# Kernel optimization log

Hardware: AMD Instinct MI355X
Metric: run time of the kernel (lower is better)

Reference implementation:

```python
import jax, jax.numpy as jnp
import numpy as np

B, S, E, H, LD, P, NC = 4, 256, 256, 8, 128, 256, 2
N = S * P  # total points (static)
EPS = 1e-5


def setup_inputs() -> dict:
    key = jax.random.key(0)
    ks = jax.random.split(key, 12)
    r = lambda i, shape, s: jax.random.normal(ks[i], shape, jnp.float32) * s
    return dict(
        gl_feats=jax.random.normal(ks[0], (S, B, E), jnp.float32),
        lo_feats=jax.random.normal(ks[1], (B, N, LD), jnp.float32),
        centroids=jax.random.normal(ks[2], (B, S, 2), jnp.float32),
        np_cluster=jnp.full((S,), P, jnp.int32),
        fc1_w=r(3, (16, 2), 0.5), fc1_b=jnp.zeros(16, jnp.float32),
        fc2_w=r(4, (E, 16), 0.1), fc2_b=jnp.zeros(E, jnp.float32),
        in_proj_w=r(5, (3 * E, E), 0.05), in_proj_b=jnp.zeros(3 * E, jnp.float32),
        out_proj_w=r(6, (E, E), 0.05), out_proj_b=jnp.zeros(E, jnp.float32),
        conv2_w=r(7, (E // 2, LD + E), 0.05), conv2_b=jnp.zeros(E // 2, jnp.float32),
        bn2_gamma=jnp.ones(E // 2, jnp.float32), bn2_beta=jnp.zeros(E // 2, jnp.float32),
        bn2_mean=jnp.zeros(E // 2, jnp.float32), bn2_var=jnp.ones(E // 2, jnp.float32),
        conv3_w=r(8, (64, E // 2), 0.05), conv3_b=jnp.zeros(64, jnp.float32),
        bn3_gamma=jnp.ones(64, jnp.float32), bn3_beta=jnp.zeros(64, jnp.float32),
        bn3_mean=jnp.zeros(64, jnp.float32), bn3_var=jnp.ones(64, jnp.float32),
        conv4_w=r(9, (NC, 64), 0.05), conv4_b=jnp.zeros(NC, jnp.float32),
    )


def _bn(z, g, b, m, v):
    # inference-mode BatchNorm1d over the channel (last) axis
    return (z - m) * jax.lax.rsqrt(v + EPS) * g + b


def reference(gl_feats, lo_feats, centroids, np_cluster,
              fc1_w, fc1_b, fc2_w, fc2_b,
              in_proj_w, in_proj_b, out_proj_w, out_proj_b,
              conv2_w, conv2_b, bn2_gamma, bn2_beta, bn2_mean, bn2_var,
              conv3_w, conv3_b, bn3_gamma, bn3_beta, bn3_mean, bn3_var,
              conv4_w, conv4_b):
    # positional encoding of centroids: Linear(2,16) -> leaky_relu -> Linear(16,E)
    h = centroids @ fc1_w.T + fc1_b                      # [B,S,16]
    h = jnp.where(h >= 0, h, 0.01 * h)                   # leaky_relu_, slope 0.01
    pos = h @ fc2_w.T + fc2_b                            # [B,S,E]
    x = gl_feats.transpose(1, 0, 2) + pos                # [B,S,E] (torch MHA is seq-first)

    # MultiheadAttention (self-attn, eval-mode dropout=identity)
    qkv = x @ in_proj_w.T + in_proj_b                    # [B,S,3E]
    q, k, v = jnp.split(qkv, 3, axis=-1)
    dh = E // H
    qh = q.reshape(B, S, H, dh)
    kh = k.reshape(B, S, H, dh)
    vh = v.reshape(B, S, H, dh)
    scores = jnp.einsum('bqhd,bkhd->bhqk', qh, kh) * (1.0 / np.sqrt(dh))
    attn = jax.nn.softmax(scores, axis=-1)               # [B,H,S,S]
    ctx = jnp.einsum('bhqk,bkhd->bqhd', attn, vh).reshape(B, S, E)
    attn_out = ctx @ out_proj_w.T + out_proj_b           # [B,S,E]

    # segment-broadcast: replace the python repeat/cat loop with a gather
    cluster_ids = jnp.repeat(jnp.arange(S), np_cluster, total_repeat_length=N)  # [N]
    global_feat = attn_out[:, cluster_ids, :]            # [B,N,E]

    pc = jnp.concatenate([lo_feats, global_feat], axis=2)  # [B,N,LD+E]
    # 1x1 Conv1d == pointwise Linear over channels
    h2 = jax.nn.relu(_bn(pc @ conv2_w.T + conv2_b, bn2_gamma, bn2_beta, bn2_mean, bn2_var))
    h3 = jax.nn.relu(_bn(h2 @ conv3_w.T + conv3_b, bn3_gamma, bn3_beta, bn3_mean, bn3_var))
    out = h3 @ conv4_w.T + conv4_b                       # [B,N,NC]
    return out.transpose(0, 2, 1)                        # [B,NC,N] to match torch layout
```

## Files before the change

### kernel.cpp

```cpp
#include <hip/hip_runtime.h>

#define B_   4
#define S_   256
#define E_   256
#define H_   8
#define LD_  128
#define N_   65536
#define NC_  2

typedef __attribute__((ext_vector_type(8))) short s8v;
typedef __attribute__((ext_vector_type(4))) float f32x4;

__device__ __forceinline__ short f2bf(float f) {
  unsigned u;
  asm("v_cvt_pk_bf16_f32 %0, %1, %2" : "=v"(u) : "v"(f), "v"(f));
  return (short)u;
}
__device__ __forceinline__ float bf2f(short s) {
  union { float f; unsigned u; } v; v.u = ((unsigned)(unsigned short)s) << 16;
  return v.f;
}
__device__ __forceinline__ s8v pack8(float4 a, float4 b) {
  union { s8v s; unsigned u[4]; } r;
  asm("v_cvt_pk_bf16_f32 %0, %1, %2" : "=v"(r.u[0]) : "v"(a.x), "v"(a.y));
  asm("v_cvt_pk_bf16_f32 %0, %1, %2" : "=v"(r.u[1]) : "v"(a.z), "v"(a.w));
  asm("v_cvt_pk_bf16_f32 %0, %1, %2" : "=v"(r.u[2]) : "v"(b.x), "v"(b.y));
  asm("v_cvt_pk_bf16_f32 %0, %1, %2" : "=v"(r.u[3]) : "v"(b.z), "v"(b.w));
  return r.s;
}

__global__ __launch_bounds__(256) void prep_k(
    const int* __restrict__ npc, int* __restrict__ ids,
    const float* __restrict__ ipw, const float* __restrict__ opw,
    const float* __restrict__ opb,
    const float* __restrict__ w2, const float* __restrict__ w3,
    const float* __restrict__ b2, const float* __restrict__ g2,
    const float* __restrict__ be2, const float* __restrict__ mu2,
    const float* __restrict__ va2,
    const float* __restrict__ b3, const float* __restrict__ g3,
    const float* __restrict__ be3, const float* __restrict__ mu3,
    const float* __restrict__ va3,
    short* __restrict__ iph, short* __restrict__ ipl,
    short* __restrict__ Mh, short* __restrict__ Ml,
    float* __restrict__ g0v,
    short* __restrict__ w2p, short* __restrict__ w3p,
    float* __restrict__ sc2, float* __restrict__ sh2,
    float* __restrict__ sc3, float* __restrict__ sh3,
    const float* __restrict__ gl, const float* __restrict__ cen,
    const float* __restrict__ fc1w, const float* __restrict__ fc1b,
    const float* __restrict__ fc2w, const float* __restrict__ fc2b,
    short* __restrict__ Xhi, short* __restrict__ Xlo) {
  __shared__ int red[256];
  __shared__ float hsh[16];
  __shared__ float wrow[256];
  __shared__ float gred[256];
  int bid = blockIdx.x, t = threadIdx.x;
  if (bid < 768) {
    int i = bid * 256 + t;
    if (i < 196608) {
      float v = ipw[i]; short h = f2bf(v);
      iph[i] = h; ipl[i] = f2bf(v - bf2f(h));
    }
    if (i < 16384) {
      int g = i >> 9, l2 = (i >> 3) & 63, j = i & 7;
      int chh = g >> 4, ct = (g >> 2) & 3, ks = g & 3;
      int row = 64 * chh + 16 * ct + (l2 & 15);
      int col = ks * 32 + (l2 >> 4) * 8 + j;
      w2p[i] = f2bf(w2[row * 384 + col]);
    }
    if (i < 8192) {
      int g = i >> 9, l2 = (i >> 3) & 63, j = i & 7;
      int ct = g >> 2, ks = g & 3;
      int row = 16 * ct + (l2 & 15);
      int col = ks * 32 + (l2 >> 4) * 8 + j;
      w3p[i] = f2bf(w3[row * 128 + col]);
    }
    if (i < 128) {
      float sc = g2[i] * rsqrtf(va2[i] + 1e-5f);
      sc2[i] = sc; sh2[i] = (b2[i] - mu2[i]) * sc + be2[i];
    }
    if (i < 64) {
      float sc = g3[i] * rsqrtf(va3[i] + 1e-5f);
      sc3[i] = sc; sh3[i] = (b3[i] - mu3[i]) * sc + be3[i];
    }
  } else if (bid <= 1024) {
    int s = bid - 768;
    int val = (s == 256) ? npc[t] : ((t < s) ? npc[t] : 0);
    red[t] = val;
    __syncthreads();
    for (int off = 128; off > 0; off >>= 1) {
      if (t < off) red[t] += red[t + off];
      __syncthreads();
    }
    int st = red[0];
    if (s < 256) {
      int en = st + npc[s]; if (en > N_) en = N_;
      for (int n = st + t; n < en; n += 256) ids[n] = s;
    } else {
      for (int n = st + t; n < N_; n += 256) ids[n] = 255;
    }
  } else if (bid <= 2048) {
    int bs = bid - 1025;
    int b = bs >> 8, s = bs & 255;
    if (t < 16) {
      float c0 = cen[bs * 2 + 0], c1 = cen[bs * 2 + 1];
      float v = c0 * fc1w[2 * t] + c1 * fc1w[2 * t + 1] + fc1b[t];
      hsh[t] = (v >= 0.f) ? v : 0.01f * v;
    }
    __syncthreads();
    float p = fc2b[t];
#pragma unroll
    for (int j = 0; j < 16; j++) p += hsh[j] * fc2w[t * 16 + j];
    float v = gl[((size_t)s * B_ + b) * E_ + t] + p;
    short h = f2bf(v);
    Xhi[(size_t)bs * E_ + t] = h;
    Xlo[(size_t)bs * E_ + t] = f2bf(v - bf2f(h));
  } else {
    int c = bid - 2049;
    wrow[t] = w2[c * 384 + 128 + t];
    gred[t] = 0.f;
    __syncthreads();
    float acc = 0.f;
#pragma unroll 8
    for (int k = 0; k < 256; k++) acc += wrow[k] * opw[(size_t)k * 256 + t];
    short h = f2bf(acc);
    Mh[(size_t)c * 256 + t] = h;
    Ml[(size_t)c * 256 + t] = f2bf(acc - bf2f(h));
    gred[t] = wrow[t] * opb[t];
    __syncthreads();
    for (int off = 128; off > 0; off >>= 1) {
      if (t < off) gred[t] += gred[t + off];
      __syncthreads();
    }
    if (t == 0) g0v[c] = gred[0];
  }
}

__global__ __launch_bounds__(256) void gemm_x3_k(
    const short* __restrict__ Ah, const short* __restrict__ Al,
    const short* __restrict__ Wh, const short* __restrict__ Wl,
    const float* __restrict__ bias, float* __restrict__ Cf,
    int M, int N, int K) {
  __shared__ __align__(16) short gs[18432];
  const int AH = 0, AL = 4608, WH = 9216, WL = 13824;
  int t = threadIdx.x;
  int row0 = blockIdx.x * 64, col0 = blockIdx.y * 64;
  int w = t >> 6, l = t & 63, quad = l >> 4, lr = l & 15;
  int m0 = w * 16;
  int ar = t >> 2, aq = (t & 3) * 16;
  f32x4 acc[4];
#pragma unroll
  for (int i = 0; i < 4; i++) acc[i] = (f32x4)(0.f);

  for (int kc = 0; kc < K; kc += 64) {
    __syncthreads();
    {
      size_t ra = (size_t)(row0 + ar) * K + kc + aq;
      size_t rw = (size_t)(col0 + ar) * K + kc + aq;
      *(s8v*)&gs[AH + ar * 72 + aq]     = *(const s8v*)&Ah[ra];
      *(s8v*)&gs[AH + ar * 72 + aq + 8] = *(const s8v*)&Ah[ra + 8];
      *(s8v*)&gs[AL + ar * 72 + aq]     = *(const s8v*)&Al[ra];
      *(s8v*)&gs[AL + ar * 72 + aq + 8] = *(const s8v*)&Al[ra + 8];
      *(s8v*)&gs[WH + ar * 72 + aq]     = *(const s8v*)&Wh[rw];
      *(s8v*)&gs[WH + ar * 72 + aq + 8] = *(const s8v*)&Wh[rw + 8];
      *(s8v*)&gs[WL + ar * 72 + aq]     = *(const s8v*)&Wl[rw];
      *(s8v*)&gs[WL + ar * 72 + aq + 8] = *(const s8v*)&Wl[rw + 8];
    }
    __syncthreads();
#pragma unroll
    for (int ks = 0; ks < 2; ks++) {
      int ko = ks * 32 + quad * 8;
      s8v ah = *(const s8v*)&gs[AH + (m0 + lr) * 72 + ko];
      s8v al = *(const s8v*)&gs[AL + (m0 + lr) * 72 + ko];
#pragma unroll
      for (int ct = 0; ct < 4; ct++) {
        s8v bh = *(const s8v*)&gs[WH + (ct * 16 + lr) * 72 + ko];
        s8v bl = *(const s8v*)&gs[WL + (ct * 16 + lr) * 72 + ko];
        acc[ct] = __builtin_amdgcn_mfma_f32_16x16x32_bf16(ah, bh, acc[ct], 0, 0, 0);
        acc[ct] = __builtin_amdgcn_mfma_f32_16x16x32_bf16(al, bh, acc[ct], 0, 0, 0);
        acc[ct] = __builtin_amdgcn_mfma_f32_16x16x32_bf16(ah, bl, acc[ct], 0, 0, 0);
      }
    }
  }
#pragma unroll
  for (int ct = 0; ct < 4; ct++) {
    int c = col0 + ct * 16 + lr;
    float bb = bias[c];
#pragma unroll
    for (int rg = 0; rg < 4; rg++) {
      int r = row0 + m0 + quad * 4 + rg;
      Cf[(size_t)r * N + c] = acc[ct][rg] + bb;
    }
  }
}

__global__ __launch_bounds__(256) void gk_k(
    const short* __restrict__ Ah, const short* __restrict__ Al,
    const short* __restrict__ Wh, const short* __restrict__ Wl,
    const float* __restrict__ g0v, float* __restrict__ G) {
  __shared__ __align__(16) short gs[13824];
  const int AH = 0, AL = 4608, WH = 9216, WL = 11520;
  int t = threadIdx.x;
  int row0 = blockIdx.x * 64, col0 = blockIdx.y * 32;
  int w = t >> 6, l = t & 63, quad = l >> 4, lr = l & 15;
  int m0 = w * 16;
  int ar = t >> 2, aq = (t & 3) * 16;
  int wr = t >> 3, wq = (t & 7) * 8;
  f32x4 acc[2];
#pragma unroll
  for (int i = 0; i < 2; i++) acc[i] = (f32x4)(0.f);

  for (int kc = 0; kc < 256; kc += 64) {
    __syncthreads();
    {
      size_t ra = (size_t)(row0 + ar) * 256 + kc + aq;
      size_t rw = (size_t)(col0 + wr) * 256 + kc + wq;
      *(s8v*)&gs[AH + ar * 72 + aq]     = *(const s8v*)&Ah[ra];
      *(s8v*)&gs[AH + ar * 72 + aq + 8] = *(const s8v*)&Ah[ra + 8];
      *(s8v*)&gs[AL + ar * 72 + aq]     = *(const s8v*)&Al[ra];
      *(s8v*)&gs[AL + ar * 72 + aq + 8] = *(const s8v*)&Al[ra + 8];
      *(s8v*)&gs[WH + wr * 72 + wq]     = *(const s8v*)&Wh[rw];
      *(s8v*)&gs[WL + wr * 72 + wq]     = *(const s8v*)&Wl[rw];
    }
    __syncthreads();
#pragma unroll
    for (int ks = 0; ks < 2; ks++) {
      int ko = ks * 32 + quad * 8;
      s8v ah = *(const s8v*)&gs[AH + (m0 + lr) * 72 + ko];
      s8v al = *(const s8v*)&gs[AL + (m0 + lr) * 72 + ko];
#pragma unroll
      for (int ct = 0; ct < 2; ct++) {
        s8v bh = *(const s8v*)&gs[WH + (ct * 16 + lr) * 72 + ko];
        s8v bl = *(const s8v*)&gs[WL + (ct * 16 + lr) * 72 + ko];
        acc[ct] = __builtin_amdgcn_mfma_f32_16x16x32_bf16(ah, bh, acc[ct], 0, 0, 0);
        acc[ct] = __builtin_amdgcn_mfma_f32_16x16x32_bf16(al, bh, acc[ct], 0, 0, 0);
        acc[ct] = __builtin_amdgcn_mfma_f32_16x16x32_bf16(ah, bl, acc[ct], 0, 0, 0);
      }
    }
  }
#pragma unroll
  for (int ct = 0; ct < 2; ct++) {
    int c = col0 + ct * 16 + lr;
    float bb = g0v[c];
#pragma unroll
    for (int rg = 0; rg < 4; rg++) {
      int r = row0 + m0 + quad * 4 + rg;
      G[(size_t)r * 128 + c] = acc[ct][rg] + bb;
    }
  }
}

__global__ __launch_bounds__(256) void attn_k(const float* __restrict__ qkv,
                                              short* __restrict__ Chi,
                                              short* __restrict__ Clo) {
  int bid = blockIdx.x;
  int qt = bid & 7, h = (bid >> 3) & 7, b = bid >> 6;
  __shared__ __align__(16) float smem[16384];
  float* Kx = smem;
  float* Vx = smem + 8192;
  int t = threadIdx.x;
#pragma unroll
  for (int i = 0; i < 8; i++) {
    int row = i * 32 + (t >> 3);
    int d4 = (t & 7) * 4;
    const float* base = qkv + (size_t)(b * S_ + row) * 768 + h * 32 + d4;
    *(float4*)&Kx[row * 32 + d4] = *(const float4*)(base + 256);
    *(float4*)&Vx[row * 32 + d4] = *(const float4*)(base + 512);
  }
  int r = t & 31, g = t >> 5;
  float q[32];
  {
    const float* qb = qkv + (size_t)(b * S_ + qt * 32 + r) * 768 + h * 32;
#pragma unroll
    for (int d4 = 0; d4 < 32; d4 += 4) {
      float4 v = *(const float4*)(qb + d4);
      q[d4] = v.x; q[d4 + 1] = v.y; q[d4 + 2] = v.z; q[d4 + 3] = v.w;
    }
  }
  __syncthreads();
  const float scale = 0.17677669529663687f;
  int kk0 = g * 32;
  float sc[32];
  float m = -1e30f;
#pragma unroll
  for (int kk = 0; kk < 32; kk++) {
    const float* kr = &Kx[(kk0 + kk) * 32];
    float4 a = (float4){0.f, 0.f, 0.f, 0.f};
#pragma unroll
    for (int d4 = 0; d4 < 32; d4 += 4) {
      float4 kv = *(const float4*)(kr + d4);
      a.x += q[d4] * kv.x; a.y += q[d4 + 1] * kv.y;
      a.z += q[d4 + 2] * kv.z; a.w += q[d4 + 3] * kv.w;
    }
    float s = ((a.x + a.y) + (a.z + a.w)) * scale;
    sc[kk] = s;
    m = fmaxf(m, s);
  }
  float lsum = 0.f;
  float ctx[32];
#pragma unroll
  for (int d = 0; d < 32; d++) ctx[d] = 0.f;
#pragma unroll
  for (int kk = 0; kk < 32; kk++) {
    const float* vr = &Vx[(kk0 + kk) * 32];
    float p = __expf(sc[kk] - m);
    lsum += p;
#pragma unroll
    for (int d4 = 0; d4 < 32; d4 += 4) {
      float4 vv = *(const float4*)(vr + d4);
      ctx[d4] += p * vv.x; ctx[d4 + 1] += p * vv.y;
      ctx[d4 + 2] += p * vv.z; ctx[d4 + 3] += p * vv.w;
    }
  }
  __syncthreads();
  float* ctxbuf = smem;
  float* mbuf = smem + 8192;
  float* lbuf = smem + 8448;
  mbuf[g * 32 + r] = m;
  lbuf[g * 32 + r] = lsum;
#pragma unroll
  for (int d = 0; d < 32; d++)
    ctxbuf[(g * 32 + r) * 32 + ((d + r) & 31)] = ctx[d];
  __syncthreads();
  int r2 = t & 31, dq = t >> 5;
  float M = -1e30f;
#pragma unroll
  for (int gg = 0; gg < 8; gg++) M = fmaxf(M, mbuf[gg * 32 + r2]);
  float wg[8]; float L = 0.f;
#pragma unroll
  for (int gg = 0; gg < 8; gg++) {
    wg[gg] = __expf(mbuf[gg * 32 + r2] - M);
    L += lbuf[gg * 32 + r2] * wg[gg];
  }
  float invL = 1.f / L;
  size_t base = (size_t)(b * S_ + qt * 32 + r2) * E_ + h * 32;
#pragma unroll
  for (int dd = 0; dd < 4; dd++) {
    int d = dq * 4 + dd;
    float o = 0.f;
#pragma unroll
    for (int gg = 0; gg < 8; gg++)
      o += ctxbuf[(gg * 32 + r2) * 32 + ((d + r2) & 31)] * wg[gg];
    o *= invL;
    short hi = f2bf(o);
    Chi[base + d] = hi;
    Clo[base + d] = f2bf(o - bf2f(hi));
  }
}

__global__ __launch_bounds__(256, 4) void conv_fused_k(
    const float* __restrict__ lo, const float* __restrict__ G,
    const int* __restrict__ ids,
    const short* __restrict__ w2p, const short* __restrict__ w3p,
    const float* __restrict__ sc2, const float* __restrict__ sh2,
    const float* __restrict__ sc3, const float* __restrict__ sh3,
    const float* __restrict__ w4, const float* __restrict__ b4,
    float* __restrict__ out) {
  __shared__ __align__(16) short smem[17408];
  __shared__ int lds_ids[128];
  int t = threadIdx.x;
  int bid = blockIdx.x;
  int b = bid >> 9;
  int n0 = (bid & 511) << 7;
  int w = t >> 6, l = t & 63;
  int quad = l >> 4, lr = l & 15;
  int mh = w & 1, chh = w >> 1;
  int ar = t >> 1, akh = (t & 1) * 64;
  const float* lob = &lo[((size_t)b * N_ + n0 + ar) * LD_ + akh];

  int id0 = ids[n0], id127 = ids[n0 + 127];
  bool uni = (id0 == id127);
  float gseed[4];
  {
    const float* gr = &G[((size_t)b * 256 + id0) * 128 + 64 * chh + lr];
#pragma unroll
    for (int ct = 0; ct < 4; ct++) gseed[ct] = gr[16 * ct];
  }
  if (t < 128) lds_ids[t] = ids[n0 + t];

  {
    float4 pf[8];
#pragma unroll
    for (int j = 0; j < 8; j++) pf[j] = *(const float4*)(lob + j * 4);
#pragma unroll
    for (int j = 0; j < 4; j++)
      *(s8v*)&smem[ar * 136 + akh + j * 8] = pack8(pf[2 * j], pf[2 * j + 1]);
#pragma unroll
    for (int j = 0; j < 8; j++) pf[j] = *(const float4*)(lob + 32 + j * 4);
#pragma unroll
    for (int j = 0; j < 4; j++)
      *(s8v*)&smem[ar * 136 + akh + 32 + j * 8] = pack8(pf[2 * j], pf[2 * j + 1]);
  }
  __syncthreads();

  f32x4 acc2[4][4];
  if (uni) {
#pragma unroll
    for (int mt = 0; mt < 4; mt++)
#pragma unroll
      for (int ct = 0; ct < 4; ct++)
#pragma unroll
        for (int rg = 0; rg < 4; rg++)
          acc2[mt][ct][rg] = gseed[ct];
  } else {
#pragma unroll
    for (int mt = 0; mt < 4; mt++)
#pragma unroll
      for (int rg = 0; rg < 4; rg++) {
        int p = 64 * mh + 16 * mt + 4 * quad + rg;
        const float* gr = &G[((size_t)b * 256 + lds_ids[p]) * 128 + 64 * chh + lr];
#pragma unroll
        for (int ct = 0; ct < 4; ct++)
          acc2[mt][ct][rg] = gr[16 * ct];
      }
  }

#pragma unroll
  for (int ks = 0; ks < 4; ks++) {
    int ko = ks * 32 + quad * 8;
    s8v af[4], bfr[4];
#pragma unroll
    for (int mt = 0; mt < 4; mt++)
      af[mt] = *(const s8v*)&smem[(64 * mh + 16 * mt + lr) * 136 + ko];
#pragma unroll
    for (int ct = 0; ct < 4; ct++)
      bfr[ct] = *(const s8v*)&w2p[(((chh * 4 + ct) * 4 + ks) << 9) + l * 8];
#pragma unroll
    for (int mt = 0; mt < 4; mt++)
#pragma unroll
      for (int ct = 0; ct < 4; ct++)
        acc2[mt][ct] = __builtin_amdgcn_mfma_f32_16x16x32_bf16(af[mt], bfr[ct], acc2[mt][ct], 0, 0, 0);
  }
  __syncthreads();

#pragma unroll
  for (int ct = 0; ct < 4; ct++) {
    int c = 64 * chh + 16 * ct + lr;
    float sc = sc2[c], sh = sh2[c];
#pragma unroll
    for (int mt = 0; mt < 4; mt++)
#pragma unroll
      for (int rg = 0; rg < 4; rg++) {
        int p = 64 * mh + 16 * mt + 4 * quad + rg;
        float z = acc2[mt][ct][rg] * sc + sh;
        smem[p * 136 + c] = f2bf(fmaxf(z, 0.f));
      }
  }
  __syncthreads();

  f32x4 acc3[2][4];
#pragma unroll
  for (int i = 0; i < 2; i++)
#pragma unroll
    for (int j = 0; j < 4; j++) acc3[i][j] = (f32x4)(0.f);
#pragma unroll
  for (int ks = 0; ks < 4; ks++) {
    int ko = ks * 32 + quad * 8;
    s8v af2[2], bf3[4];
#pragma unroll
    for (int mt = 0; mt < 2; mt++)
      af2[mt] = *(const s8v*)&smem[(32 * w + 16 * mt + lr) * 136 + ko];
#pragma unroll
    for (int ct = 0; ct < 4; ct++)
      bf3[ct] = *(const s8v*)&w3p[(((ct * 4) + ks) << 9) + l * 8];
#pragma unroll
    for (int mt = 0; mt < 2; mt++)
#pragma unroll
      for (int ct = 0; ct < 4; ct++)
        acc3[mt][ct] = __builtin_amdgcn_mfma_f32_16x16x32_bf16(af2[mt], bf3[ct], acc3[mt][ct], 0, 0, 0);
  }

  float w4c0[4], w4c1[4], s3[4], b3sh[4];
#pragma unroll
  for (int ct = 0; ct < 4; ct++) {
    int c = 16 * ct + lr;
    s3[ct] = sc3[c]; b3sh[ct] = sh3[c];
    w4c0[ct] = w4[c];
    w4c1[ct] = w4[64 + c];
  }
  int c4s = lr & 1, rgs = (lr >> 1) & 3, mts = lr >> 3;
  float myout = 0.f;
#pragma unroll
  for (int mt = 0; mt < 2; mt++)
#pragma unroll
    for (int rg = 0; rg < 4; rg++) {
      float p0 = 0.f, p1 = 0.f;
#pragma unroll
      for (int ct = 0; ct < 4; ct++) {
        float z = fmaxf(fmaf(acc3[mt][ct][rg], s3[ct], b3sh[ct]), 0.f);
        p0 = fmaf(z, w4c0[ct], p0);
        p1 = fmaf(z, w4c1[ct], p1);
      }
#pragma unroll
      for (int m = 1; m < 16; m <<= 1) {
        p0 += __shfl_xor(p0, m, 64);
        p1 += __shfl_xor(p1, m, 64);
      }
      bool mine = (mt == mts) && (rg == rgs);
      float pv = c4s ? p1 : p0;
      myout = mine ? pv : myout;
    }
  {
    int p = 32 * w + 16 * mts + 4 * quad + rgs;
    out[((size_t)b * NC_ + c4s) * N_ + n0 + p] = myout + b4[c4s];
  }
}

extern "C" void kernel_launch(void* const* d_in, const int* in_sizes, int n_in,
                              void* d_out, int out_size, void* d_ws, size_t ws_size,
                              hipStream_t stream) {
  const float* gl   = (const float*)d_in[0];
  const float* lo   = (const float*)d_in[1];
  const float* cen  = (const float*)d_in[2];
  const int*   npc  = (const int*)d_in[3];
  const float* fc1w = (const float*)d_in[4];
  const float* fc1b = (const float*)d_in[5];
  const float* fc2w = (const float*)d_in[6];
  const float* fc2b = (const float*)d_in[7];
  const float* ipw  = (const float*)d_in[8];
  const float* ipb  = (const float*)d_in[9];
  const float* opw  = (const float*)d_in[10];
  const float* opb  = (const float*)d_in[11];
  const float* w2   = (const float*)d_in[12];
  const float* b2   = (const float*)d_in[13];
  const float* g2   = (const float*)d_in[14];
  const float* be2  = (const float*)d_in[15];
  const float* mu2  = (const float*)d_in[16];
  const float* va2  = (const float*)d_in[17];
  const float* w3   = (const float*)d_in[18];
  const float* b3   = (const float*)d_in[19];
  const float* g3   = (const float*)d_in[20];
  const float* be3  = (const float*)d_in[21];
  const float* mu3  = (const float*)d_in[22];
  const float* va3  = (const float*)d_in[23];
  const float* w4   = (const float*)d_in[24];
  const float* b4   = (const float*)d_in[25];

  char* ws = (char*)d_ws;
  float* qkv  = (float*)(ws);
  short* Xhi  = (short*)(ws + 3145728);
  short* Xlo  = (short*)(ws + 3670016);
  short* Chi  = (short*)(ws + 4194304);
  short* Clo  = (short*)(ws + 4718592);
  float* G    = (float*)(ws + 5242880);
  short* iph  = (short*)(ws + 5767168);
  short* ipl  = (short*)(ws + 6160384);
  short* Mh   = (short*)(ws + 6553600);
  short* Ml   = (short*)(ws + 6684672);
  short* w2p  = (short*)(ws + 6815744);
  short* w3p  = (short*)(ws + 6914048);
  int*   ids  = (int*)  (ws + 6930432);
  float* sc2  = (float*)(ws + 7192576);
  float* sh2  = (float*)(ws + 7193088);
  float* sc3  = (float*)(ws + 7193600);
  float* sh3  = (float*)(ws + 7193856);
  float* g0v  = (float*)(ws + 7194112);
  float* out  = (float*)d_out;

  prep_k<<<2177, 256, 0, stream>>>(npc, ids, ipw, opw, opb, w2, w3,
                                   b2, g2, be2, mu2, va2,
                                   b3, g3, be3, mu3, va3,
                                   iph, ipl, Mh, Ml, g0v, w2p, w3p,
                                   sc2, sh2, sc3, sh3,
                                   gl, cen, fc1w, fc1b, fc2w, fc2b, Xhi, Xlo);
  gemm_x3_k<<<dim3(16, 12), 256, 0, stream>>>(Xhi, Xlo, iph, ipl, ipb,
                                              qkv, B_ * S_, 768, E_);
  attn_k<<<B_ * H_ * 8, 256, 0, stream>>>(qkv, Chi, Clo);
  gk_k<<<dim3(16, 4), 256, 0, stream>>>(Chi, Clo, Mh, Ml, g0v, G);
  conv_fused_k<<<B_ * (N_ / 128), 256, 0, stream>>>(
      lo, G, ids, w2p, w3p, sc2, sh2, sc3, sh3, w4, b4, out);
}
```

Measured before the change: 301.1 us.

## Fuse global-feature projection into conv kernel and drop separate gk kernel

Removes the gk_k launch and instead has each conv_fused_k block recompute its cluster's projected global feature (128 dot products over 256 elements) from the hi/lo bf16 context and weight splits. A scalar per-point fallback handles blocks that straddle cluster boundaries. The qkv GEMM is switched to the narrower 64x32 tile with twice as many column blocks. This trades one kernel launch and the G round-trip for redundant per-block work and extra L2 reads of the Mh/Ml weights across 2048 blocks.

```diff
diff --git a/kernel.cpp b/kernel.cpp
--- a/kernel.cpp
+++ b/kernel.cpp
@@ -141,63 +141,6 @@
     const short* __restrict__ Wh, const short* __restrict__ Wl,
     const float* __restrict__ bias, float* __restrict__ Cf,
     int M, int N, int K) {
-  __shared__ __align__(16) short gs[18432];
-  const int AH = 0, AL = 4608, WH = 9216, WL = 13824;
-  int t = threadIdx.x;
-  int row0 = blockIdx.x * 64, col0 = blockIdx.y * 64;
-  int w = t >> 6, l = t & 63, quad = l >> 4, lr = l & 15;
-  int m0 = w * 16;
-  int ar = t >> 2, aq = (t & 3) * 16;
-  f32x4 acc[4];
-#pragma unroll
-  for (int i = 0; i < 4; i++) acc[i] = (f32x4)(0.f);
-
-  for (int kc = 0; kc < K; kc += 64) {
-    __syncthreads();
-    {
-      size_t ra = (size_t)(row0 + ar) * K + kc + aq;
-      size_t rw = (size_t)(col0 + ar) * K + kc + aq;
-      *(s8v*)&gs[AH + ar * 72 + aq]     = *(const s8v*)&Ah[ra];
-      *(s8v*)&gs[AH + ar * 72 + aq + 8] = *(const s8v*)&Ah[ra + 8];
-      *(s8v*)&gs[AL + ar * 72 + aq]     = *(const s8v*)&Al[ra];
-      *(s8v*)&gs[AL + ar * 72 + aq + 8] = *(const s8v*)&Al[ra + 8];
-      *(s8v*)&gs[WH + ar * 72 + aq]     = *(const s8v*)&Wh[rw];
-      *(s8v*)&gs[WH + ar * 72 + aq + 8] = *(const s8v*)&Wh[rw + 8];
-      *(s8v*)&gs[WL + ar * 72 + aq]     = *(const s8v*)&Wl[rw];
-      *(s8v*)&gs[WL + ar * 72 + aq + 8] = *(const s8v*)&Wl[rw + 8];
-    }
-    __syncthreads();
-#pragma unroll
-    for (int ks = 0; ks < 2; ks++) {
-      int ko = ks * 32 + quad * 8;
-      s8v ah = *(const s8v*)&gs[AH + (m0 + lr) * 72 + ko];
-      s8v al = *(const s8v*)&gs[AL + (m0 + lr) * 72 + ko];
-#pragma unroll
-      for (int ct = 0; ct < 4; ct++) {
-        s8v bh = *(const s8v*)&gs[WH + (ct * 16 + lr) * 72 + ko];
-        s8v bl = *(const s8v*)&gs[WL + (ct * 16 + lr) * 72 + ko];
-        acc[ct] = __builtin_amdgcn_mfma_f32_16x16x32_bf16(ah, bh, acc[ct], 0, 0, 0);
-        acc[ct] = __builtin_amdgcn_mfma_f32_16x16x32_bf16(al, bh, acc[ct], 0, 0, 0);
-        acc[ct] = __builtin_amdgcn_mfma_f32_16x16x32_bf16(ah, bl, acc[ct], 0, 0, 0);
-      }
-    }
-  }
-#pragma unroll
-  for (int ct = 0; ct < 4; ct++) {
-    int c = col0 + ct * 16 + lr;
-    float bb = bias[c];
-#pragma unroll
-    for (int rg = 0; rg < 4; rg++) {
-      int r = row0 + m0 + quad * 4 + rg;
-      Cf[(size_t)r * N + c] = acc[ct][rg] + bb;
-    }
-  }
-}
-
-__global__ __launch_bounds__(256) void gk_k(
-    const short* __restrict__ Ah, const short* __restrict__ Al,
-    const short* __restrict__ Wh, const short* __restrict__ Wl,
-    const float* __restrict__ g0v, float* __restrict__ G) {
   __shared__ __align__(16) short gs[13824];
   const int AH = 0, AL = 4608, WH = 9216, WL = 11520;
   int t = threadIdx.x;
@@ -210,11 +153,11 @@
 #pragma unroll
   for (int i = 0; i < 2; i++) acc[i] = (f32x4)(0.f);
 
-  for (int kc = 0; kc < 256; kc += 64) {
+  for (int kc = 0; kc < K; kc += 64) {
     __syncthreads();
     {
-      size_t ra = (size_t)(row0 + ar) * 256 + kc + aq;
-      size_t rw = (size_t)(col0 + wr) * 256 + kc + wq;
+      size_t ra = (size_t)(row0 + ar) * K + kc + aq;
+      size_t rw = (size_t)(col0 + wr) * K + kc + wq;
       *(s8v*)&gs[AH + ar * 72 + aq]     = *(const s8v*)&Ah[ra];
       *(s8v*)&gs[AH + ar * 72 + aq + 8] = *(const s8v*)&Ah[ra + 8];
       *(s8v*)&gs[AL + ar * 72 + aq]     = *(const s8v*)&Al[ra];
@@ -241,11 +184,11 @@
 #pragma unroll
   for (int ct = 0; ct < 2; ct++) {
     int c = col0 + ct * 16 + lr;
-    float bb = g0v[c];
+    float bb = bias[c];
 #pragma unroll
     for (int rg = 0; rg < 4; rg++) {
       int r = row0 + m0 + quad * 4 + rg;
-      G[(size_t)r * 128 + c] = acc[ct][rg] + bb;
+      Cf[(size_t)r * N + c] = acc[ct][rg] + bb;
     }
   }
 }
@@ -349,7 +292,10 @@
 }
 
 __global__ __launch_bounds__(256, 4) void conv_fused_k(
-    const float* __restrict__ lo, const float* __restrict__ G,
+    const float* __restrict__ lo,
+    const short* __restrict__ Chi, const short* __restrict__ Clo,
+    const short* __restrict__ Mh, const short* __restrict__ Ml,
+    const float* __restrict__ g0v,
     const int* __restrict__ ids,
     const short* __restrict__ w2p, const short* __restrict__ w3p,
     const float* __restrict__ sc2, const float* __restrict__ sh2,
@@ -358,6 +304,7 @@
     float* __restrict__ out) {
   __shared__ __align__(16) short smem[17408];
   __shared__ int lds_ids[128];
+  __shared__ float gbuf[128];
   int t = threadIdx.x;
   int bid = blockIdx.x;
   int b = bid >> 9;
@@ -370,12 +317,6 @@
 
   int id0 = ids[n0], id127 = ids[n0 + 127];
   bool uni = (id0 == id127);
-  float gseed[4];
-  {
-    const float* gr = &G[((size_t)b * 256 + id0) * 128 + 64 * chh + lr];
-#pragma unroll
-    for (int ct = 0; ct < 4; ct++) gseed[ct] = gr[16 * ct];
-  }
   if (t < 128) lds_ids[t] = ids[n0 + t];
 
   {
@@ -391,10 +332,32 @@
     for (int j = 0; j < 4; j++)
       *(s8v*)&smem[ar * 136 + akh + 32 + j * 8] = pack8(pf[2 * j], pf[2 * j + 1]);
   }
+
+  if (t < 128) {
+    const short* chp = &Chi[((size_t)(b * 256 + id0)) * 256];
+    const short* clp = &Clo[((size_t)(b * 256 + id0)) * 256];
+    const short* mhp = &Mh[(size_t)t * 256];
+    const short* mlp = &Ml[(size_t)t * 256];
+    float s = g0v[t];
+#pragma unroll 4
+    for (int e = 0; e < 256; e += 8) {
+      s8v cv = *(const s8v*)&chp[e];
+      s8v lv = *(const s8v*)&clp[e];
+      s8v mv = *(const s8v*)&mhp[e];
+      s8v nv = *(const s8v*)&mlp[e];
+#pragma unroll
+      for (int j = 0; j < 8; j++)
+        s += (bf2f(cv[j]) + bf2f(lv[j])) * (bf2f(mv[j]) + bf2f(nv[j]));
+    }
+    gbuf[t] = s;
+  }
   __syncthreads();
 
   f32x4 acc2[4][4];
   if (uni) {
+    float gseed[4];
+#pragma unroll
+    for (int ct = 0; ct < 4; ct++) gseed[ct] = gbuf[64 * chh + 16 * ct + lr];
 #pragma unroll
     for (int mt = 0; mt < 4; mt++)
 #pragma unroll
@@ -403,15 +366,21 @@
         for (int rg = 0; rg < 4; rg++)
           acc2[mt][ct][rg] = gseed[ct];
   } else {
-#pragma unroll
     for (int mt = 0; mt < 4; mt++)
-#pragma unroll
       for (int rg = 0; rg < 4; rg++) {
         int p = 64 * mh + 16 * mt + 4 * quad + rg;
-        const float* gr = &G[((size_t)b * 256 + lds_ids[p]) * 128 + 64 * chh + lr];
-#pragma unroll
-        for (int ct = 0; ct < 4; ct++)
-          acc2[mt][ct][rg] = gr[16 * ct];
+        int id = lds_ids[p];
+        const short* chp = &Chi[((size_t)(b * 256 + id)) * 256];
+        const short* clp = &Clo[((size_t)(b * 256 + id)) * 256];
+        for (int ct = 0; ct < 4; ct++) {
+          int c = 64 * chh + 16 * ct + lr;
+          const short* mhp = &Mh[(size_t)c * 256];
+          const short* mlp = &Ml[(size_t)c * 256];
+          float s = g0v[c];
+          for (int e = 0; e < 256; e++)
+            s += (bf2f(chp[e]) + bf2f(clp[e])) * (bf2f(mhp[e]) + bf2f(mlp[e]));
+          acc2[mt][ct][rg] = s;
+        }
       }
   }
 
@@ -542,7 +511,6 @@
   short* Xlo  = (short*)(ws + 3670016);
   short* Chi  = (short*)(ws + 4194304);
   short* Clo  = (short*)(ws + 4718592);
-  float* G    = (float*)(ws + 5242880);
   short* iph  = (short*)(ws + 5767168);
   short* ipl  = (short*)(ws + 6160384);
   short* Mh   = (short*)(ws + 6553600);
@@ -563,10 +531,10 @@
                                    iph, ipl, Mh, Ml, g0v, w2p, w3p,
                                    sc2, sh2, sc3, sh3,
                                    gl, cen, fc1w, fc1b, fc2w, fc2b, Xhi, Xlo);
-  gemm_x3_k<<<dim3(16, 12), 256, 0, stream>>>(Xhi, Xlo, iph, ipl, ipb,
+  gemm_x3_k<<<dim3(16, 24), 256, 0, stream>>>(Xhi, Xlo, iph, ipl, ipb,
                                               qkv, B_ * S_, 768, E_);
   attn_k<<<B_ * H_ * 8, 256, 0, stream>>>(qkv, Chi, Clo);
-  gk_k<<<dim3(16, 4), 256, 0, stream>>>(Chi, Clo, Mh, Ml, g0v, G);
   conv_fused_k<<<B_ * (N_ / 128), 256, 0, stream>>>(
-      lo, G, ids, w2p, w3p, sc2, sh2, sc3, sh3, w4, b4, out);
-}
+      lo, Chi, Clo, Mh, Ml, g0v, ids, w2p, w3p,
+      sc2, sh2, sc3, sh3, w4, b4, out);
+}
```

New measurement: 328.4 us. 9.1% more time.
